# Optimization experiments

Measured on AMD Instinct MI355X. Metric: run time of the kernel, lower is better.

Reference implementation:

```python
import jax
import jax.numpy as jnp
from jax import lax
import numpy as np

BATCH, SEQ, STATES = 64, 4096, 64


def setup_inputs() -> dict:
    key = jax.random.key(0)
    k1, k2, k3, k4 = jax.random.split(key, 4)
    scores = jax.random.normal(k1, (BATCH, SEQ, STATES), dtype=jnp.float32)
    transition = jax.random.normal(k2, (STATES, STATES), dtype=jnp.float32)
    source = jax.random.uniform(k3, (STATES,), dtype=jnp.float32)
    sink = jax.random.uniform(k4, (STATES,), dtype=jnp.float32)
    return {"scores": scores, "transition": transition, "source": source, "sink": sink}


def reference(scores, transition, source, sink):
    # Linear-chain CRF log-partition (forward algorithm in log space).
    # scores: (B, T, S) emission scores; transition: (S, S) [from, to].
    B, T, S = scores.shape
    # t == 0: original code logsumexps a broadcast-identical axis of size S,
    # which adds a constant log(S) -- reproduced here for bit-faithful math.
    score0 = source[None, :] + scores[:, 0] + jnp.log(jnp.asarray(S, scores.dtype))  # (B, S)

    def step(alpha, s_t):
        # alpha: (B, S) log-scores over previous state; s_t: (B, S) emissions at t
        new = jax.nn.logsumexp(alpha[:, :, None] + transition[None, :, :], axis=1) + s_t
        return new, None

    # scan over time: (T-1, B, S)
    alpha_final, _ = lax.scan(step, score0, jnp.swapaxes(scores[:, 1:], 0, 1))
    return jax.nn.logsumexp(alpha_final + sink[None, :], axis=1)  # (B,)
```

## Files before the change

### kernel.cpp

```cpp
#include <hip/hip_runtime.h>
#include <cstdint>


#define B_    64
#define T_    4096
#define S_    64
#define L_    15
#define NC_   273
#define WPB_  18
#define CPB_  288
#define LOG2E 1.44269504088896340736f

typedef float  f32x4  __attribute__((ext_vector_type(4)));
typedef __bf16 bf16x8 __attribute__((ext_vector_type(8)));
union U4B { uint4 u; bf16x8 b; };

__device__ __forceinline__ unsigned rne_bf16(float f) {
    unsigned x = __float_as_uint(f);
    return (x + 0x7FFFu + ((x >> 16) & 1u)) >> 16;
}
__device__ __forceinline__ unsigned pk2(float a, float b) {
    return rne_bf16(a) | (rne_bf16(b) << 16);
}

__global__ __launch_bounds__(64, 3) void crf_phase1(
    const float* __restrict__ scores,
    const float* __restrict__ transition,
    float* __restrict__ Ybuf, float* __restrict__ Zbuf, float* __restrict__ Lz)
{
    __shared__ float tb[2][16][68];
    const int wid  = blockIdx.x;
    const bool bwd = wid >= (B_ * WPB_);
    const int wl   = bwd ? wid - B_ * WPB_ : wid;
    const int b    = wl / WPB_, wg = wl % WPB_;
    const int lane = threadIdx.x, g = lane >> 4, l = lane & 15;

    bf16x8 BE[2][4];
    #pragma unroll
    for (int kb = 0; kb < 2; ++kb)
    #pragma unroll
    for (int nt = 0; nt < 4; ++nt) {
        unsigned pk[4];
        #pragma unroll
        for (int dd = 0; dd < 4; ++dd) {
            int k0 = 32 * kb + 8 * g + 2 * dd, n = 16 * nt + l;
            float e0, e1;
            if (!bwd) { e0 = transition[k0 * 64 + n]; e1 = transition[(k0 + 1) * 64 + n]; }
            else      { e0 = transition[n * 64 + k0]; e1 = transition[n * 64 + k0 + 1]; }
            pk[dd] = pk2(exp2f(e0 * LOG2E), exp2f(e1 * LOG2E));
        }
        U4B t; t.u = make_uint4(pk[0], pk[1], pk[2], pk[3]); BE[kb][nt] = t.b;
    }

    int cl = 16 * wg + l; if (cl > NC_ - 1) cl = NC_ - 1;
    const float* ap = scores + ((size_t)b * T_ + 15 * cl + (bwd ? 15 : 0)) * S_ + 8 * g;

    f32x4 acc[4];
    int Lt[4] = {0, 0, 0, 0};

    auto mfma8 = [&](bf16x8 A0, bf16x8 A1) {
        #pragma unroll
        for (int nt = 0; nt < 4; ++nt) {
            f32x4 z4 = {0.f, 0.f, 0.f, 0.f};
            z4      = __builtin_amdgcn_mfma_f32_16x16x32_bf16(A0, BE[0][nt], z4, 0, 0, 0);
            acc[nt] = __builtin_amdgcn_mfma_f32_16x16x32_bf16(A1, BE[1][nt], z4, 0, 0, 0);
        }
    };
    auto renorm = [&]() {
        #pragma unroll
        for (int r = 0; r < 4; ++r) {
            float m = fmaxf(fmaxf(acc[0][r], acc[1][r]), fmaxf(acc[2][r], acc[3][r]));
            m = fmaxf(m, __shfl_xor(m, 1, 64));
            m = fmaxf(m, __shfl_xor(m, 2, 64));
            m = fmaxf(m, __shfl_xor(m, 4, 64));
            m = fmaxf(m, __shfl_xor(m, 8, 64));
            int ex = (int)(__float_as_uint(m) >> 23) - 127;
            float sc = __uint_as_float((unsigned)(127 - ex) << 23);
            Lt[r] += ex;
            #pragma unroll
            for (int nt = 0; nt < 4; ++nt) acc[nt][r] *= sc;
        }
    };
    auto xposeA = [&](int par, const f32x4& c0, const f32x4& c1,
                      const f32x4& c2, const f32x4& c3, bf16x8& A0, bf16x8& A1) {
        float (*tp)[68] = tb[par];
        #pragma unroll
        for (int nt = 0; nt < 4; ++nt)
            #pragma unroll
            for (int r = 0; r < 4; ++r)
                tp[4 * g + r][16 * nt + l] = acc[nt][r];
        __builtin_amdgcn_s_waitcnt(0xC07F);
        __builtin_amdgcn_wave_barrier();
        const float* rowp = &tp[l][8 * g];
        f32x4 x0 = *(const f32x4*)rowp;
        f32x4 x1 = *(const f32x4*)(rowp + 4);
        f32x4 x2 = *(const f32x4*)(rowp + 32);
        f32x4 x3 = *(const f32x4*)(rowp + 36);
        U4B t0, t1;
        t0.u.x = pk2(x0[0] * exp2f(c0[0] * LOG2E), x0[1] * exp2f(c0[1] * LOG2E));
        t0.u.y = pk2(x0[2] * exp2f(c0[2] * LOG2E), x0[3] * exp2f(c0[3] * LOG2E));
        t0.u.z = pk2(x1[0] * exp2f(c1[0] * LOG2E), x1[1] * exp2f(c1[1] * LOG2E));
        t0.u.w = pk2(x1[2] * exp2f(c1[2] * LOG2E), x1[3] * exp2f(c1[3] * LOG2E));
        t1.u.x = pk2(x2[0] * exp2f(c2[0] * LOG2E), x2[1] * exp2f(c2[1] * LOG2E));
        t1.u.y = pk2(x2[2] * exp2f(c2[2] * LOG2E), x2[3] * exp2f(c2[3] * LOG2E));
        t1.u.z = pk2(x3[0] * exp2f(c3[0] * LOG2E), x3[1] * exp2f(c3[1] * LOG2E));
        t1.u.w = pk2(x3[2] * exp2f(c3[2] * LOG2E), x3[3] * exp2f(c3[3] * LOG2E));
        A0 = t0.b; A1 = t1.b;
    };
    auto ldq = [&](int idx, f32x4& q0, f32x4& q1, f32x4& q2, f32x4& q3) {
        const float* p = ap + (ptrdiff_t)idx * S_;
        q0 = *(const f32x4*)p;        q1 = *(const f32x4*)(p + 4);
        q2 = *(const f32x4*)(p + 32); q3 = *(const f32x4*)(p + 36);
    };

    if (!bwd) {
        f32x4 q0, q1, q2, q3;
        ldq(1, q0, q1, q2, q3);
        { U4B t; t.u = make_uint4(0x3F803F80u, 0x3F803F80u, 0x3F803F80u, 0x3F803F80u);
          mfma8(t.b, t.b); }
        #pragma unroll 2
        for (int tt = 1; tt < L_; ++tt) {
            f32x4 c0 = q0, c1 = q1, c2 = q2, c3 = q3;
            if (tt + 1 < L_) ldq(tt + 1, q0, q1, q2, q3);
            bf16x8 A0, A1;
            xposeA(tt & 1, c0, c1, c2, c3, A0, A1);
            mfma8(A0, A1);
            if ((tt & 3) == 3) renorm();
        }
        #pragma unroll
        for (int r = 0; r < 4; ++r) {
            int c = 16 * wg + 4 * g + r; int cc = c > NC_ - 1 ? NC_ - 1 : c;
            const float* bp = scores + ((size_t)b * T_ + 15 * cc + 15) * S_ + l;
            float* yb = Ybuf + ((size_t)b * CPB_ + c) * S_ + l;
            #pragma unroll
            for (int nt = 0; nt < 4; ++nt)
                yb[16 * nt] = acc[nt][r] * exp2f(bp[16 * nt] * LOG2E);
        }
    } else {
        f32x4 q0, q1, q2, q3, n0, n1, n2, n3;
        ldq(0, q0, q1, q2, q3);
        ldq(-1, n0, n1, n2, n3);
        {
            U4B t0, t1;
            t0.u.x = pk2(exp2f(q0[0] * LOG2E), exp2f(q0[1] * LOG2E));
            t0.u.y = pk2(exp2f(q0[2] * LOG2E), exp2f(q0[3] * LOG2E));
            t0.u.z = pk2(exp2f(q1[0] * LOG2E), exp2f(q1[1] * LOG2E));
            t0.u.w = pk2(exp2f(q1[2] * LOG2E), exp2f(q1[3] * LOG2E));
            t1.u.x = pk2(exp2f(q2[0] * LOG2E), exp2f(q2[1] * LOG2E));
            t1.u.y = pk2(exp2f(q2[2] * LOG2E), exp2f(q2[3] * LOG2E));
            t1.u.z = pk2(exp2f(q3[0] * LOG2E), exp2f(q3[1] * LOG2E));
            t1.u.w = pk2(exp2f(q3[2] * LOG2E), exp2f(q3[3] * LOG2E));
            mfma8(t0.b, t1.b);
        }
        #pragma unroll 2
        for (int i = 1; i < L_; ++i) {
            f32x4 c0 = n0, c1 = n1, c2 = n2, c3 = n3;
            if (i + 1 < L_) ldq(-(i + 1), n0, n1, n2, n3);
            bf16x8 A0, A1;
            xposeA(i & 1, c0, c1, c2, c3, A0, A1);
            mfma8(A0, A1);
            if ((i & 3) == 3) renorm();
        }
        #pragma unroll
        for (int r = 0; r < 4; ++r) {
            int c = 16 * wg + 4 * g + r;
            float* zb = Zbuf + ((size_t)b * CPB_ + c) * S_ + l;
            #pragma unroll
            for (int nt = 0; nt < 4; ++nt) zb[16 * nt] = acc[nt][r];
            if (l == 0) Lz[b * CPB_ + c] = (float)Lt[r];
        }
    }
}

__global__ __launch_bounds__(512) void crf_phase2(
    const float* __restrict__ scores, const float* __restrict__ source,
    const float* __restrict__ sink,
    const float* __restrict__ Ybuf, const float* __restrict__ Zbuf,
    const float* __restrict__ Lz, float* __restrict__ out)
{
    __shared__ float part[8];
    const int b = blockIdx.x;
    const int wv = threadIdx.x >> 6, lane = threadIdx.x & 63;
    const float esink = exp2f(sink[lane] * LOG2E);

    float acc = 0.f;
    for (int c = wv; c < NC_; c += 8) {
        float yh = Ybuf[((size_t)b * CPB_ + c) * 64 + lane];
        float nx = (c < NC_ - 1) ? Zbuf[((size_t)b * CPB_ + c + 1) * 64 + lane] : esink;
        float p = yh * nx, q = yh;
        #pragma unroll
        for (int m = 32; m >= 1; m >>= 1) {
            p += __shfl_xor(p, m, 64);
            q += __shfl_xor(q, m, 64);
        }
        acc += log2f(p) - log2f(q) + Lz[b * CPB_ + c];
    }
    if (wv == 0) {
        float a0 = exp2f((source[lane] + scores[(size_t)b * T_ * S_ + lane]) * LOG2E);
        float p = a0 * Zbuf[((size_t)b * CPB_) * 64 + lane];
        #pragma unroll
        for (int m = 32; m >= 1; m >>= 1) p += __shfl_xor(p, m, 64);
        acc += log2f(p);
    }
    if (lane == 0) part[wv] = acc;
    __syncthreads();
    if (threadIdx.x == 0) {
        float s = 0.f;
        #pragma unroll
        for (int i = 0; i < 8; ++i) s += part[i];
        out[b] = 0.6931471805599453f * s + 4.158883083359672f;
    }
}

extern "C" void kernel_launch(void* const* d_in, const int* in_sizes, int n_in,
                              void* d_out, int out_size, void* d_ws, size_t ws_size,
                              hipStream_t stream) {
    (void)in_sizes; (void)n_in; (void)out_size; (void)ws_size;
    const float* scores     = (const float*)d_in[0];
    const float* transition = (const float*)d_in[1];
    const float* source     = (const float*)d_in[2];
    const float* sink       = (const float*)d_in[3];
    float* out = (float*)d_out;

    float* Ybuf = (float*)d_ws;
    float* Zbuf = Ybuf + (size_t)B_ * CPB_ * 64;
    float* Lz   = Zbuf + (size_t)B_ * CPB_ * 64;

    hipLaunchKernelGGL(crf_phase1, dim3(2 * B_ * WPB_), dim3(64), 0, stream,
                       scores, transition, Ybuf, Zbuf, Lz);
    hipLaunchKernelGGL(crf_phase2, dim3(B_), dim3(512), 0, stream,
                       scores, source, sink, Ybuf, Zbuf, Lz, out);
}
```

Baseline: 138.0 us.

## Shrink time chunks to 5 steps, drop renormalisation, double occupancy

Splits the sequence into 819 chunks of 5 steps instead of 273 chunks of 15. This shortens each wave's serial dependency chain and launches three times as many waves, with launch bounds raised to 6 waves per SIMD. With chunks this short, the exponent-tracking renormalisation and its Lz buffer are removed, and the LDS transpose buffer is no longer double-buffered. bf16 packing now uses compiler conversions, and phase 2 uses 16 waves to reduce the larger chunk count. The cost is more workspace traffic and more partial reductions in phase 2, plus a risk of overflow or underflow without renormalisation if the scores drift.

Result: slower. 196.1 us (+42.1%).

```diff
diff --git a/kernel.cpp b/kernel.cpp
--- a/kernel.cpp
+++ b/kernel.cpp
@@ -5,30 +5,22 @@
 #define B_    64
 #define T_    4096
 #define S_    64
-#define L_    15
-#define NC_   273
-#define WPB_  18
-#define CPB_  288
+#define L_    5
+#define NC_   819
+#define WPB_  52
+#define CPB_  832
 #define LOG2E 1.44269504088896340736f
 
 typedef float  f32x4  __attribute__((ext_vector_type(4)));
 typedef __bf16 bf16x8 __attribute__((ext_vector_type(8)));
 union U4B { uint4 u; bf16x8 b; };
 
-__device__ __forceinline__ unsigned rne_bf16(float f) {
-    unsigned x = __float_as_uint(f);
-    return (x + 0x7FFFu + ((x >> 16) & 1u)) >> 16;
-}
-__device__ __forceinline__ unsigned pk2(float a, float b) {
-    return rne_bf16(a) | (rne_bf16(b) << 16);
-}
-
-__global__ __launch_bounds__(64, 3) void crf_phase1(
+__global__ __launch_bounds__(64, 6) void crf_phase1(
     const float* __restrict__ scores,
     const float* __restrict__ transition,
-    float* __restrict__ Ybuf, float* __restrict__ Zbuf, float* __restrict__ Lz)
+    float* __restrict__ Ybuf, float* __restrict__ Zbuf)
 {
-    __shared__ float tb[2][16][68];
+    __shared__ float tb[16][68];
     const int wid  = blockIdx.x;
     const bool bwd = wid >= (B_ * WPB_);
     const int wl   = bwd ? wid - B_ * WPB_ : wid;
@@ -40,23 +32,23 @@
     for (int kb = 0; kb < 2; ++kb)
     #pragma unroll
     for (int nt = 0; nt < 4; ++nt) {
-        unsigned pk[4];
+        bf16x8 t;
         #pragma unroll
         for (int dd = 0; dd < 4; ++dd) {
             int k0 = 32 * kb + 8 * g + 2 * dd, n = 16 * nt + l;
             float e0, e1;
             if (!bwd) { e0 = transition[k0 * 64 + n]; e1 = transition[(k0 + 1) * 64 + n]; }
             else      { e0 = transition[n * 64 + k0]; e1 = transition[n * 64 + k0 + 1]; }
-            pk[dd] = pk2(exp2f(e0 * LOG2E), exp2f(e1 * LOG2E));
-        }
-        U4B t; t.u = make_uint4(pk[0], pk[1], pk[2], pk[3]); BE[kb][nt] = t.b;
+            t[2 * dd]     = (__bf16)exp2f(e0 * LOG2E);
+            t[2 * dd + 1] = (__bf16)exp2f(e1 * LOG2E);
+        }
+        BE[kb][nt] = t;
     }
 
     int cl = 16 * wg + l; if (cl > NC_ - 1) cl = NC_ - 1;
-    const float* ap = scores + ((size_t)b * T_ + 15 * cl + (bwd ? 15 : 0)) * S_ + 8 * g;
+    const float* ap = scores + ((size_t)b * T_ + L_ * cl + (bwd ? L_ : 0)) * S_ + 8 * g;
 
     f32x4 acc[4];
-    int Lt[4] = {0, 0, 0, 0};
 
     auto mfma8 = [&](bf16x8 A0, bf16x8 A1) {
         #pragma unroll
@@ -66,46 +58,27 @@
             acc[nt] = __builtin_amdgcn_mfma_f32_16x16x32_bf16(A1, BE[1][nt], z4, 0, 0, 0);
         }
     };
-    auto renorm = [&]() {
-        #pragma unroll
-        for (int r = 0; r < 4; ++r) {
-            float m = fmaxf(fmaxf(acc[0][r], acc[1][r]), fmaxf(acc[2][r], acc[3][r]));
-            m = fmaxf(m, __shfl_xor(m, 1, 64));
-            m = fmaxf(m, __shfl_xor(m, 2, 64));
-            m = fmaxf(m, __shfl_xor(m, 4, 64));
-            m = fmaxf(m, __shfl_xor(m, 8, 64));
-            int ex = (int)(__float_as_uint(m) >> 23) - 127;
-            float sc = __uint_as_float((unsigned)(127 - ex) << 23);
-            Lt[r] += ex;
-            #pragma unroll
-            for (int nt = 0; nt < 4; ++nt) acc[nt][r] *= sc;
-        }
-    };
-    auto xposeA = [&](int par, const f32x4& c0, const f32x4& c1,
+    auto xposeA = [&](const f32x4& c0, const f32x4& c1,
                       const f32x4& c2, const f32x4& c3, bf16x8& A0, bf16x8& A1) {
-        float (*tp)[68] = tb[par];
         #pragma unroll
         for (int nt = 0; nt < 4; ++nt)
             #pragma unroll
             for (int r = 0; r < 4; ++r)
-                tp[4 * g + r][16 * nt + l] = acc[nt][r];
+                tb[4 * g + r][16 * nt + l] = acc[nt][r];
         __builtin_amdgcn_s_waitcnt(0xC07F);
         __builtin_amdgcn_wave_barrier();
-        const float* rowp = &tp[l][8 * g];
+        const float* rowp = &tb[l][8 * g];
         f32x4 x0 = *(const f32x4*)rowp;
         f32x4 x1 = *(const f32x4*)(rowp + 4);
         f32x4 x2 = *(const f32x4*)(rowp + 32);
         f32x4 x3 = *(const f32x4*)(rowp + 36);
-        U4B t0, t1;
-        t0.u.x = pk2(x0[0] * exp2f(c0[0] * LOG2E), x0[1] * exp2f(c0[1] * LOG2E));
-        t0.u.y = pk2(x0[2] * exp2f(c0[2] * LOG2E), x0[3] * exp2f(c0[3] * LOG2E));
-        t0.u.z = pk2(x1[0] * exp2f(c1[0] * LOG2E), x1[1] * exp2f(c1[1] * LOG2E));
-        t0.u.w = pk2(x1[2] * exp2f(c1[2] * LOG2E), x1[3] * exp2f(c1[3] * LOG2E));
-        t1.u.x = pk2(x2[0] * exp2f(c2[0] * LOG2E), x2[1] * exp2f(c2[1] * LOG2E));
-        t1.u.y = pk2(x2[2] * exp2f(c2[2] * LOG2E), x2[3] * exp2f(c2[3] * LOG2E));
-        t1.u.z = pk2(x3[0] * exp2f(c3[0] * LOG2E), x3[1] * exp2f(c3[1] * LOG2E));
-        t1.u.w = pk2(x3[2] * exp2f(c3[2] * LOG2E), x3[3] * exp2f(c3[3] * LOG2E));
-        A0 = t0.b; A1 = t1.b;
+        #pragma unroll
+        for (int d = 0; d < 4; ++d) {
+            A0[d]     = (__bf16)(x0[d] * exp2f(c0[d] * LOG2E));
+            A0[d + 4] = (__bf16)(x1[d] * exp2f(c1[d] * LOG2E));
+            A1[d]     = (__bf16)(x2[d] * exp2f(c2[d] * LOG2E));
+            A1[d + 4] = (__bf16)(x3[d] * exp2f(c3[d] * LOG2E));
+        }
     };
     auto ldq = [&](int idx, f32x4& q0, f32x4& q1, f32x4& q2, f32x4& q3) {
         const float* p = ap + (ptrdiff_t)idx * S_;
@@ -118,19 +91,18 @@
         ldq(1, q0, q1, q2, q3);
         { U4B t; t.u = make_uint4(0x3F803F80u, 0x3F803F80u, 0x3F803F80u, 0x3F803F80u);
           mfma8(t.b, t.b); }
-        #pragma unroll 2
+        #pragma unroll
         for (int tt = 1; tt < L_; ++tt) {
             f32x4 c0 = q0, c1 = q1, c2 = q2, c3 = q3;
             if (tt + 1 < L_) ldq(tt + 1, q0, q1, q2, q3);
             bf16x8 A0, A1;
-            xposeA(tt & 1, c0, c1, c2, c3, A0, A1);
+            xposeA(c0, c1, c2, c3, A0, A1);
             mfma8(A0, A1);
-            if ((tt & 3) == 3) renorm();
         }
         #pragma unroll
         for (int r = 0; r < 4; ++r) {
             int c = 16 * wg + 4 * g + r; int cc = c > NC_ - 1 ? NC_ - 1 : c;
-            const float* bp = scores + ((size_t)b * T_ + 15 * cc + 15) * S_ + l;
+            const float* bp = scores + ((size_t)b * T_ + L_ * cc + L_) * S_ + l;
             float* yb = Ybuf + ((size_t)b * CPB_ + c) * S_ + l;
             #pragma unroll
             for (int nt = 0; nt < 4; ++nt)
@@ -141,25 +113,23 @@
         ldq(0, q0, q1, q2, q3);
         ldq(-1, n0, n1, n2, n3);
         {
-            U4B t0, t1;
-            t0.u.x = pk2(exp2f(q0[0] * LOG2E), exp2f(q0[1] * LOG2E));
-            t0.u.y = pk2(exp2f(q0[2] * LOG2E), exp2f(q0[3] * LOG2E));
-            t0.u.z = pk2(exp2f(q1[0] * LOG2E), exp2f(q1[1] * LOG2E));
-            t0.u.w = pk2(exp2f(q1[2] * LOG2E), exp2f(q1[3] * LOG2E));
-            t1.u.x = pk2(exp2f(q2[0] * LOG2E), exp2f(q2[1] * LOG2E));
-            t1.u.y = pk2(exp2f(q2[2] * LOG2E), exp2f(q2[3] * LOG2E));
-            t1.u.z = pk2(exp2f(q3[0] * LOG2E), exp2f(q3[1] * LOG2E));
-            t1.u.w = pk2(exp2f(q3[2] * LOG2E), exp2f(q3[3] * LOG2E));
-            mfma8(t0.b, t1.b);
-        }
-        #pragma unroll 2
+            bf16x8 A0, A1;
+            #pragma unroll
+            for (int d = 0; d < 4; ++d) {
+                A0[d]     = (__bf16)exp2f(q0[d] * LOG2E);
+                A0[d + 4] = (__bf16)exp2f(q1[d] * LOG2E);
+                A1[d]     = (__bf16)exp2f(q2[d] * LOG2E);
+                A1[d + 4] = (__bf16)exp2f(q3[d] * LOG2E);
+            }
+            mfma8(A0, A1);
+        }
+        #pragma unroll
         for (int i = 1; i < L_; ++i) {
             f32x4 c0 = n0, c1 = n1, c2 = n2, c3 = n3;
             if (i + 1 < L_) ldq(-(i + 1), n0, n1, n2, n3);
             bf16x8 A0, A1;
-            xposeA(i & 1, c0, c1, c2, c3, A0, A1);
+            xposeA(c0, c1, c2, c3, A0, A1);
             mfma8(A0, A1);
-            if ((i & 3) == 3) renorm();
         }
         #pragma unroll
         for (int r = 0; r < 4; ++r) {
@@ -167,24 +137,23 @@
             float* zb = Zbuf + ((size_t)b * CPB_ + c) * S_ + l;
             #pragma unroll
             for (int nt = 0; nt < 4; ++nt) zb[16 * nt] = acc[nt][r];
-            if (l == 0) Lz[b * CPB_ + c] = (float)Lt[r];
         }
     }
 }
 
-__global__ __launch_bounds__(512) void crf_phase2(
+__global__ __launch_bounds__(1024) void crf_phase2(
     const float* __restrict__ scores, const float* __restrict__ source,
     const float* __restrict__ sink,
     const float* __restrict__ Ybuf, const float* __restrict__ Zbuf,
-    const float* __restrict__ Lz, float* __restrict__ out)
+    float* __restrict__ out)
 {
-    __shared__ float part[8];
+    __shared__ float part[16];
     const int b = blockIdx.x;
     const int wv = threadIdx.x >> 6, lane = threadIdx.x & 63;
     const float esink = exp2f(sink[lane] * LOG2E);
 
     float acc = 0.f;
-    for (int c = wv; c < NC_; c += 8) {
+    for (int c = wv; c < NC_; c += 16) {
         float yh = Ybuf[((size_t)b * CPB_ + c) * 64 + lane];
         float nx = (c < NC_ - 1) ? Zbuf[((size_t)b * CPB_ + c + 1) * 64 + lane] : esink;
         float p = yh * nx, q = yh;
@@ -193,7 +162,7 @@
             p += __shfl_xor(p, m, 64);
             q += __shfl_xor(q, m, 64);
         }
-        acc += log2f(p) - log2f(q) + Lz[b * CPB_ + c];
+        acc += log2f(p) - log2f(q);
     }
     if (wv == 0) {
         float a0 = exp2f((source[lane] + scores[(size_t)b * T_ * S_ + lane]) * LOG2E);
@@ -207,7 +176,7 @@
     if (threadIdx.x == 0) {
         float s = 0.f;
         #pragma unroll
-        for (int i = 0; i < 8; ++i) s += part[i];
+        for (int i = 0; i < 16; ++i) s += part[i];
         out[b] = 0.6931471805599453f * s + 4.158883083359672f;
     }
 }
@@ -224,10 +193,9 @@
 
     float* Ybuf = (float*)d_ws;
     float* Zbuf = Ybuf + (size_t)B_ * CPB_ * 64;
-    float* Lz   = Zbuf + (size_t)B_ * CPB_ * 64;
 
     hipLaunchKernelGGL(crf_phase1, dim3(2 * B_ * WPB_), dim3(64), 0, stream,
-                       scores, transition, Ybuf, Zbuf, Lz);
-    hipLaunchKernelGGL(crf_phase2, dim3(B_), dim3(512), 0, stream,
-                       scores, source, sink, Ybuf, Zbuf, Lz, out);
+                       scores, transition, Ybuf, Zbuf);
+    hipLaunchKernelGGL(crf_phase2, dim3(B_), dim3(1024), 0, stream,
+                       scores, source, sink, Ybuf, Zbuf, out);
 }
```
